# Optimization experiments

Hardware: AMD Instinct MI355X
Metric: run time of the kernel (lower is better)

Reference implementation:

```python
import jax, jax.numpy as jnp
import numpy as np

MAXDIS = 1e-3   # squared-distance threshold for edge acceptance
COUNT = 5       # interpolation points per segment
EPS_ABS = 1e-5  # added per-coordinate before sqrt in vector norm


def setup_inputs() -> dict:
    key = jax.random.key(0)
    k1, k2 = jax.random.split(key)
    recon_points = jax.random.uniform(k1, (16, 17, 2), dtype=jnp.float32)
    gt_points = jax.random.uniform(k2, (16, 4096, 2), dtype=jnp.float32)
    return {"recon_points": recon_points, "gt_points": gt_points}


def _edge_mask(p1, p2):
    # For every keypoint pair (i, j), sample COUNT points on the segment
    # start=p1[:,i], end=p1[:,j]:  K = start*t + end*(1-t), t in linspace(0,1,COUNT).
    B, N, D = p1.shape
    t = jnp.linspace(0.0, 1.0, COUNT).astype(p1.dtype)          # [C]
    K = (p1[:, :, None, None, :] * t[None, None, None, :, None]
         + p1[:, None, :, None, :] * (1.0 - t)[None, None, None, :, None])  # [B,N,N,C,D]
    # Squared distances to gt points via ||K||^2 + ||p2||^2 - 2 K.p2^T (avoids [.,.,M,D] blowup)
    k2 = jnp.sum(K * K, axis=-1)                                  # [B,N,N,C]
    g2 = jnp.sum(p2 * p2, axis=-1)                                # [B,M]
    cross = jnp.einsum('bijcd,bmd->bijcm', K, p2)                 # [B,N,N,C,M]
    d2 = k2[..., None] + g2[:, None, None, None, :] - 2.0 * cross
    cdis = jnp.mean(jnp.min(d2, axis=-1), axis=-1)                # [B,N,N]: mean over C of min over M
    # Edges only for i > j (original loops j in range(i)); squared-dist threshold.
    tril = jnp.tril(jnp.ones((N, N), dtype=bool), k=-1)
    return (cdis < MAXDIS) & tril[None, :, :]                     # [B,N,N]


def reference(recon_points, gt_points):
    p1, p2 = recon_points, gt_points
    B, N, D = p1.shape
    mask = _edge_mask(p1, p2).astype(p1.dtype)                    # [B,N,N]
    # Flattened vector index k<N corresponds to pair (0, k): u_k = p1[:,0] - p1[:,k].
    u = p1[:, :1, :] - p1                                         # [B,N,D]
    dot = jnp.abs(jnp.einsum('bid,bjd->bij', u, u))               # [B,N,N]
    absu = jnp.sqrt(jnp.sum(u * u + EPS_ABS, axis=-1))            # [B,N]  (= sqrt(||u||^2 + D*eps))
    abs_dot = absu[:, :, None] * absu[:, None, :]                 # [B,N,N]
    abs_dot = jnp.where(abs_dot == 0, jnp.ones_like(abs_dot), abs_dot)
    cos = dot * mask / abs_dot
    idx_num = 1.0 + jnp.sum(mask)                                 # 1 + total edge count
    return jnp.sum(cos) / idx_num
```

## Files before the change

kernel.cpp:

```cpp
#include <hip/hip_runtime.h>
#include <math.h>

#define BATCH 16
#define NPTS 17
#define MPTS 4096
#define NPAIR 136
#define NPAIRS_TOTAL (BATCH * NPAIR)
#define NBLK (NPAIRS_TOTAL / 4)
#define CNT 5
#define MAXDIS 1e-3f
#define EPS_ABS 1e-5f

__global__ __launch_bounds__(256) void pair_kernel(const float* __restrict__ recon,
                                                   const float* __restrict__ gt,
                                                   float2* __restrict__ slots) {
    const int wave = threadIdx.x >> 6;
    const int lane = threadIdx.x & 63;
    const int wv = blockIdx.x * 4 + wave;
    const int b = wv / NPAIR;
    const int p = wv - b * NPAIR;
    int i = 1;
    while ((i * (i + 1)) / 2 <= p) ++i;
    const int j = p - (i * (i - 1)) / 2;

    const float* rp = recon + b * NPTS * 2;
    const float pix = rp[2 * i], piy = rp[2 * i + 1];
    const float pjx = rp[2 * j], pjy = rp[2 * j + 1];

    const float ex = pix - pjx, ey = piy - pjy;
    const float e2x = 2.0f * ex, e2y = 2.0f * ey;
    const float E = ex * ex + ey * ey;

    float ms0 = 1e30f, ms1 = 1e30f, ms2 = 1e30f, ms3 = 1e30f, ms4 = 1e30f;

    const float4* g4 = (const float4*)(gt + (size_t)b * MPTS * 2);
    #pragma unroll 4
    for (int q = lane; q < MPTS / 2; q += 64) {
        const float4 g = g4[q];
        const float dxa = pjx - g.x, dya = pjy - g.y;
        const float Aa = fmaf(dxa, dxa, dya * dya);
        const float Ba = fmaf(e2x, dxa, e2y * dya);
        const float dxb = pjx - g.z, dyb = pjy - g.w;
        const float Ab = fmaf(dxb, dxb, dyb * dyb);
        const float Bb = fmaf(e2x, dxb, e2y * dyb);

        ms0 = fminf(ms0, fminf(Aa, Ab));
        ms1 = fminf(ms1, fminf(fmaf(0.25f, Ba, Aa), fmaf(0.25f, Bb, Ab)));
        ms2 = fminf(ms2, fminf(fmaf(0.50f, Ba, Aa), fmaf(0.50f, Bb, Ab)));
        ms3 = fminf(ms3, fminf(fmaf(0.75f, Ba, Aa), fmaf(0.75f, Bb, Ab)));
        ms4 = fminf(ms4, fminf(Aa + Ba, Ab + Bb));
    }

    #pragma unroll
    for (int off = 32; off > 0; off >>= 1) {
        ms0 = fminf(ms0, __shfl_xor(ms0, off, 64));
        ms1 = fminf(ms1, __shfl_xor(ms1, off, 64));
        ms2 = fminf(ms2, __shfl_xor(ms2, off, 64));
        ms3 = fminf(ms3, __shfl_xor(ms3, off, 64));
        ms4 = fminf(ms4, __shfl_xor(ms4, off, 64));
    }

    __shared__ float2 part[4];
    if (lane == 0) {
        const float m0 = ms0;
        const float m1 = fmaf(0.0625f, E, ms1);
        const float m2 = fmaf(0.25f, E, ms2);
        const float m3 = fmaf(0.5625f, E, ms3);
        const float m4 = ms4 + E;
        const float cdis = ((((m0 + m1) + m2) + m3) + m4) / 5.0f;
        float cosv = 0.0f, cntv = 0.0f;
        if (cdis < MAXDIS) {
            const float u0x = rp[0], u0y = rp[1];
            const float uix = u0x - pix, uiy = u0y - piy;
            const float ujx = u0x - pjx, ujy = u0y - pjy;
            const float dot = fabsf(uix * ujx + uiy * ujy);
            const float ai = sqrtf((uix * uix + EPS_ABS) + (uiy * uiy + EPS_ABS));
            const float aj = sqrtf((ujx * ujx + EPS_ABS) + (ujy * ujy + EPS_ABS));
            cosv = dot / (ai * aj);
            cntv = 1.0f;
        }
        part[wave] = make_float2(cosv, cntv);
    }
    __syncthreads();
    if (threadIdx.x == 0) {
        const float2 a = part[0], bb = part[1], cc = part[2], dd = part[3];
        slots[blockIdx.x] = make_float2(((a.x + bb.x) + cc.x) + dd.x,
                                        ((a.y + bb.y) + cc.y) + dd.y);
    }
}

__global__ __launch_bounds__(64) void reduce_kernel(const float2* __restrict__ slots,
                                                    float* __restrict__ out) {
    const int lane = threadIdx.x;
    float c = 0.0f, n = 0.0f;
    #pragma unroll
    for (int m = 0; m < 9; ++m) {
        const int k = lane + 64 * m;
        if (k < NBLK) {
            const float2 w = slots[k];
            c += w.x;
            n += w.y;
        }
    }
    #pragma unroll
    for (int off = 32; off > 0; off >>= 1) {
        c += __shfl_xor(c, off, 64);
        n += __shfl_xor(n, off, 64);
    }
    if (lane == 0) out[0] = c / (1.0f + n);
}

extern "C" void kernel_launch(void* const* d_in, const int* in_sizes, int n_in,
                              void* d_out, int out_size, void* d_ws, size_t ws_size,
                              hipStream_t stream) {
    const float* recon = (const float*)d_in[0];
    const float* gt = (const float*)d_in[1];
    float* out = (float*)d_out;
    float2* slots = (float2*)d_ws;

    pair_kernel<<<NBLK, 256, 0, stream>>>(recon, gt, slots);
    reduce_kernel<<<1, 64, 0, stream>>>(slots, out);
}
```

Before: 15.31 us.

## Assign one block per keypoint pair and split gt points across four waves

Each 256-thread block now handles a single (batch, pair) instead of four pairs, one per wave. The 4096 gt points are split across all four waves, each lane doing 8 float4 loads. Per-wave minima are combined through shared memory before thread 0 computes the threshold and cosine. This raises the grid from 544 to 2176 blocks to improve parallelism and shorten each wave's serial loop, at the cost of more blocks, a cross-wave min step, and a larger final reduction (2176 slots).

Result: faster. 13.23 us (median of 2 runs) (-13.6%).

```diff
diff --git a/kernel.cpp b/kernel.cpp
--- a/kernel.cpp
+++ b/kernel.cpp
@@ -6,7 +6,6 @@
 #define MPTS 4096
 #define NPAIR 136
 #define NPAIRS_TOTAL (BATCH * NPAIR)
-#define NBLK (NPAIRS_TOTAL / 4)
 #define CNT 5
 #define MAXDIS 1e-3f
 #define EPS_ABS 1e-5f
@@ -14,11 +13,11 @@
 __global__ __launch_bounds__(256) void pair_kernel(const float* __restrict__ recon,
                                                    const float* __restrict__ gt,
                                                    float2* __restrict__ slots) {
+    const int blk = blockIdx.x;
     const int wave = threadIdx.x >> 6;
     const int lane = threadIdx.x & 63;
-    const int wv = blockIdx.x * 4 + wave;
-    const int b = wv / NPAIR;
-    const int p = wv - b * NPAIR;
+    const int b = blk / NPAIR;
+    const int p = blk - b * NPAIR;
     int i = 1;
     while ((i * (i + 1)) / 2 <= p) ++i;
     const int j = p - (i * (i - 1)) / 2;
@@ -34,9 +33,9 @@
     float ms0 = 1e30f, ms1 = 1e30f, ms2 = 1e30f, ms3 = 1e30f, ms4 = 1e30f;
 
     const float4* g4 = (const float4*)(gt + (size_t)b * MPTS * 2);
-    #pragma unroll 4
-    for (int q = lane; q < MPTS / 2; q += 64) {
-        const float4 g = g4[q];
+    #pragma unroll
+    for (int it = 0; it < 8; ++it) {
+        const float4 g = g4[threadIdx.x + (it << 8)];
         const float dxa = pjx - g.x, dya = pjy - g.y;
         const float Aa = fmaf(dxa, dxa, dya * dya);
         const float Ba = fmaf(e2x, dxa, e2y * dya);
@@ -60,14 +59,29 @@
         ms4 = fminf(ms4, __shfl_xor(ms4, off, 64));
     }
 
-    __shared__ float2 part[4];
+    __shared__ float part[4][CNT];
     if (lane == 0) {
-        const float m0 = ms0;
-        const float m1 = fmaf(0.0625f, E, ms1);
-        const float m2 = fmaf(0.25f, E, ms2);
-        const float m3 = fmaf(0.5625f, E, ms3);
-        const float m4 = ms4 + E;
+        part[wave][0] = ms0;
+        part[wave][1] = ms1;
+        part[wave][2] = ms2;
+        part[wave][3] = ms3;
+        part[wave][4] = ms4;
+    }
+    __syncthreads();
+
+    if (threadIdx.x == 0) {
+        float m[CNT];
+        #pragma unroll
+        for (int c = 0; c < CNT; ++c)
+            m[c] = fminf(fminf(part[0][c], part[1][c]),
+                         fminf(part[2][c], part[3][c]));
+        const float m0 = m[0];
+        const float m1 = fmaf(0.0625f, E, m[1]);
+        const float m2 = fmaf(0.25f, E, m[2]);
+        const float m3 = fmaf(0.5625f, E, m[3]);
+        const float m4 = m[4] + E;
         const float cdis = ((((m0 + m1) + m2) + m3) + m4) / 5.0f;
+
         float cosv = 0.0f, cntv = 0.0f;
         if (cdis < MAXDIS) {
             const float u0x = rp[0], u0y = rp[1];
@@ -79,13 +93,7 @@
             cosv = dot / (ai * aj);
             cntv = 1.0f;
         }
-        part[wave] = make_float2(cosv, cntv);
-    }
-    __syncthreads();
-    if (threadIdx.x == 0) {
-        const float2 a = part[0], bb = part[1], cc = part[2], dd = part[3];
-        slots[blockIdx.x] = make_float2(((a.x + bb.x) + cc.x) + dd.x,
-                                        ((a.y + bb.y) + cc.y) + dd.y);
+        slots[blk] = make_float2(cosv, cntv);
     }
 }
 
@@ -94,13 +102,10 @@
     const int lane = threadIdx.x;
     float c = 0.0f, n = 0.0f;
     #pragma unroll
-    for (int m = 0; m < 9; ++m) {
-        const int k = lane + 64 * m;
-        if (k < NBLK) {
-            const float2 w = slots[k];
-            c += w.x;
-            n += w.y;
-        }
+    for (int m = 0; m < NPAIRS_TOTAL / 64; ++m) {
+        const float2 w = slots[lane + 64 * m];
+        c += w.x;
+        n += w.y;
     }
     #pragma unroll
     for (int off = 32; off > 0; off >>= 1) {
@@ -118,6 +123,6 @@
     float* out = (float*)d_out;
     float2* slots = (float2*)d_ws;
 
-    pair_kernel<<<NBLK, 256, 0, stream>>>(recon, gt, slots);
+    pair_kernel<<<NPAIRS_TOTAL, 256, 0, stream>>>(recon, gt, slots);
     reduce_kernel<<<1, 64, 0, stream>>>(slots, out);
 }
```
